# Kernel tuning notes

Hardware: AMD Instinct MI355X
Metric: run time of the kernel (lower is better)

## Reference

```python
import jax, jax.numpy as jnp
import numpy as np

SELF_LOOP_EPS = 0.5

def setup_inputs() -> dict:
    key = jax.random.key(0)
    k1, k2 = jax.random.split(key)
    spatial_nodes = jax.random.normal(k1, (16, 2048, 64), dtype=jnp.float32)
    temporal_nodes = jax.random.normal(k2, (16, 64, 64), dtype=jnp.float32)
    return {"spatial_nodes": spatial_nodes, "temporal_nodes": temporal_nodes}

def reference(spatial_nodes, temporal_nodes):
    # concat spatial and temporal node embeddings along the node axis: [B, N+T, D]
    node_embs = jnp.concatenate([spatial_nodes, temporal_nodes], axis=1)
    # batched gram matrix: [B, M, M], M = N+T
    adj = jnp.einsum('bnf,bmf->bnm', node_embs, node_embs)
    adj = jnp.tanh(jax.nn.relu(adj))
    M = adj.shape[1]
    # add scaled self loops
    adj = adj + jnp.eye(M, dtype=adj.dtype) * SELF_LOOP_EPS
    # the torch module additionally extracts per-batch nonzero (edge_index, edge_weight)
    # lists; that is data-dependent stream compaction. The dense adj (plus its nonzero
    # mask) carries the identical information in a jit-compatible fixed-shape form.
    return adj
```

## Files before the change

### kernel.cpp

```cpp
#include <hip/hip_runtime.h>
#include <hip/hip_fp16.h>


#define B_BATCH   16
#define N_SPATIAL 2048
#define T_TEMP    64
#define M_NODES   2112
#define D_FEAT    64
#define TILE      64
#define LDSK      72

#define GROUPS_PER_STRIP 17
#define WGS_PER_BATCH    (33 * GROUPS_PER_STRIP)
#define TOTAL_WGS        (WGS_PER_BATCH * B_BATCH)
#define WGS_PER_XCD      (TOTAL_WGS / 8)

typedef _Float16 f16x8 __attribute__((ext_vector_type(8)));
typedef float    f32x4 __attribute__((ext_vector_type(4)));

__device__ __forceinline__ f16x8 cvt2(const float4* p) {
    float4 a = p[0], c = p[1];
    f16x8 h;
    h[0] = (_Float16)a.x; h[1] = (_Float16)a.y;
    h[2] = (_Float16)a.z; h[3] = (_Float16)a.w;
    h[4] = (_Float16)c.x; h[5] = (_Float16)c.y;
    h[6] = (_Float16)c.z; h[7] = (_Float16)c.w;
    return h;
}

__global__ __launch_bounds__(256, 4)
void gram_tanh_mfma(const float* __restrict__ sp,
                    const float* __restrict__ tp,
                    float* __restrict__ out)
{
    const int lin = blockIdx.x;
    const int xcd = lin & 7;
    const int l   = lin >> 3;
    const int bo  = l / WGS_PER_BATCH;
    const int rr  = l - bo * WGS_PER_BATCH;
    const int ti  = rr / GROUPS_PER_STRIP;
    const int g   = rr - ti * GROUPS_PER_STRIP;
    const int b   = 2 * xcd + bo;
    const int tj0 = 2 * g;
    const bool have2 = (tj0 + 1 < 33);
    const int tj1 = have2 ? tj0 + 1 : 32;

    __shared__ __align__(16) _Float16 As[TILE][LDSK];
    __shared__ __align__(16) _Float16 Bs[2][TILE][LDSK];

    const int tid = threadIdx.x;

    {
        const int row = tid >> 2;
        const int kb  = (tid & 3) * 16;
        const float* srcA = (ti < 32)
            ? sp + ((size_t)b * N_SPATIAL + (size_t)ti * TILE) * D_FEAT
            : tp + (size_t)b * T_TEMP * D_FEAT;
        const float* srcB0 = (tj0 < 32)
            ? sp + ((size_t)b * N_SPATIAL + (size_t)tj0 * TILE) * D_FEAT
            : tp + (size_t)b * T_TEMP * D_FEAT;
        const float* srcB1 = (tj1 < 32)
            ? sp + ((size_t)b * N_SPATIAL + (size_t)tj1 * TILE) * D_FEAT
            : tp + (size_t)b * T_TEMP * D_FEAT;
        const float4* pa  = (const float4*)(srcA  + (size_t)row * D_FEAT + kb);
        const float4* pb0 = (const float4*)(srcB0 + (size_t)row * D_FEAT + kb);
        const float4* pb1 = (const float4*)(srcB1 + (size_t)row * D_FEAT + kb);

        *(f16x8*)&As[row][kb]        = cvt2(pa);
        *(f16x8*)&As[row][kb + 8]    = cvt2(pa + 2);
        *(f16x8*)&Bs[0][row][kb]     = cvt2(pb0);
        *(f16x8*)&Bs[0][row][kb + 8] = cvt2(pb0 + 2);
        *(f16x8*)&Bs[1][row][kb]     = cvt2(pb1);
        *(f16x8*)&Bs[1][row][kb + 8] = cvt2(pb1 + 2);
    }
    __syncthreads();

    const int wave = tid >> 6;
    const int lane = tid & 63;
    const int lr   = lane & 15;
    const int q    = lane >> 4;

    f32x4 acc[2][4];
    #pragma unroll
    for (int n = 0; n < 2; ++n)
        #pragma unroll
        for (int tt = 0; tt < 4; ++tt) acc[n][tt] = (f32x4){0.f, 0.f, 0.f, 0.f};

    #pragma unroll
    for (int s = 0; s < 2; ++s) {
        f16x8 afrag = *(const f16x8*)&As[wave * 16 + lr][s * 32 + q * 8];
        #pragma unroll
        for (int n = 0; n < 2; ++n) {
            #pragma unroll
            for (int tt = 0; tt < 4; ++tt) {
                f16x8 bfrag = *(const f16x8*)&Bs[n][tt * 16 + lr][s * 32 + q * 8];
                acc[n][tt] = __builtin_amdgcn_mfma_f32_16x16x32_f16(bfrag, afrag, acc[n][tt], 0, 0, 0);
            }
        }
    }

    #pragma unroll
    for (int n = 0; n < 2; ++n) {
        if (n == 1 && !have2) break;
        const int tjn = n ? tj1 : tj0;
        const bool diagT = (ti == tjn);
        const int r_loc = wave * 16 + lr;
        float* dst = out + (size_t)b * M_NODES * M_NODES
                         + (size_t)(ti * TILE + r_loc) * M_NODES
                         + (size_t)(tjn * TILE + q * 4);
        #pragma unroll
        for (int tt = 0; tt < 4; ++tt) {
            const int c_loc = tt * 16 + q * 4;
            float4 o;
            float* po = &o.x;
            #pragma unroll
            for (int i = 0; i < 4; ++i) {
                float x = fmaxf(acc[n][tt][i], 0.f);
                float e = __expf(2.f * x);
                float v = 1.f - 2.f * __builtin_amdgcn_rcpf(e + 1.f);
                if (diagT && (r_loc == c_loc + i)) v += 0.5f;
                po[i] = v;
            }
            *(float4*)(dst + tt * 16) = o;
        }
    }
}

extern "C" void kernel_launch(void* const* d_in, const int* in_sizes, int n_in,
                              void* d_out, int out_size, void* d_ws, size_t ws_size,
                              hipStream_t stream) {
    const float* sp = (const float*)d_in[0];
    const float* tp = (const float*)d_in[1];
    float* out = (float*)d_out;

    dim3 grid(TOTAL_WGS);
    dim3 block(256);
    hipLaunchKernelGGL(gram_tanh_mfma, grid, block, 0, stream, sp, tp, out);
}
```

Baseline: 290.6 us.

## Exploit Gram symmetry: compute upper-triangle tiles and mirror-write transposes

Remaps the grid so each batch launches only the workgroups covering the upper triangle of 64x64 tile pairs (305 instead of 561). Each off-diagonal tile is computed once and written twice: once directly, and once transposed via a second MFMA with swapped operands. This halves the global loads of input tiles and the number of workgroups, while the output write volume stays the same. The extra MFMAs and the uneven per-workgroup work (mirror tiles do double the stores) add cost in exchange, on a kernel that is mostly bound by output writes.

```diff
diff --git a/kernel.cpp b/kernel.cpp
--- a/kernel.cpp
+++ b/kernel.cpp
@@ -10,10 +10,10 @@
 #define TILE      64
 #define LDSK      72
 
-#define GROUPS_PER_STRIP 17
-#define WGS_PER_BATCH    (33 * GROUPS_PER_STRIP)
-#define TOTAL_WGS        (WGS_PER_BATCH * B_BATCH)
-#define WGS_PER_XCD      (TOTAL_WGS / 8)
+#define WGS_PER_BATCH 305
+#define TRI_BASE      272
+#define TOTAL_WGS     (WGS_PER_BATCH * B_BATCH)
+#define WGS_PER_XCD   (TOTAL_WGS / 8)
 
 typedef _Float16 f16x8 __attribute__((ext_vector_type(8)));
 typedef float    f32x4 __attribute__((ext_vector_type(4)));
@@ -28,6 +28,12 @@
     return h;
 }
 
+__device__ __forceinline__ float tanh_relu(float x) {
+    x = fmaxf(x, 0.f);
+    float e = __expf(2.f * x);
+    return 1.f - 2.f * __builtin_amdgcn_rcpf(e + 1.f);
+}
+
 __global__ __launch_bounds__(256, 4)
 void gram_tanh_mfma(const float* __restrict__ sp,
                     const float* __restrict__ tp,
@@ -36,14 +42,23 @@
     const int lin = blockIdx.x;
     const int xcd = lin & 7;
     const int l   = lin >> 3;
-    const int bo  = l / WGS_PER_BATCH;
-    const int rr  = l - bo * WGS_PER_BATCH;
-    const int ti  = rr / GROUPS_PER_STRIP;
-    const int g   = rr - ti * GROUPS_PER_STRIP;
+    const int bo  = (l >= WGS_PER_BATCH) ? 1 : 0;
+    const int t   = l - bo * WGS_PER_BATCH;
     const int b   = 2 * xcd + bo;
-    const int tj0 = 2 * g;
+
+    int c2, r;
+    if (t >= TRI_BASE) { c2 = 16; r = t - TRI_BASE; }
+    else {
+        c2 = (int)(0.5f * (sqrtf((float)(4 * t + 1)) - 1.f));
+        while ((c2 + 1) * (c2 + 2) <= t) ++c2;
+        while (c2 * (c2 + 1) > t) --c2;
+        r = t - c2 * (c2 + 1);
+    }
+    const int ti  = r;
+    const int tj0 = 2 * c2;
     const bool have2 = (tj0 + 1 < 33);
     const int tj1 = have2 ? tj0 + 1 : 32;
+    const bool do0 = (tj0 >= ti);
 
     __shared__ __align__(16) _Float16 As[TILE][LDSK];
     __shared__ __align__(16) _Float16 Bs[2][TILE][LDSK];
@@ -56,22 +71,26 @@
         const float* srcA = (ti < 32)
             ? sp + ((size_t)b * N_SPATIAL + (size_t)ti * TILE) * D_FEAT
             : tp + (size_t)b * T_TEMP * D_FEAT;
-        const float* srcB0 = (tj0 < 32)
-            ? sp + ((size_t)b * N_SPATIAL + (size_t)tj0 * TILE) * D_FEAT
-            : tp + (size_t)b * T_TEMP * D_FEAT;
-        const float* srcB1 = (tj1 < 32)
-            ? sp + ((size_t)b * N_SPATIAL + (size_t)tj1 * TILE) * D_FEAT
-            : tp + (size_t)b * T_TEMP * D_FEAT;
-        const float4* pa  = (const float4*)(srcA  + (size_t)row * D_FEAT + kb);
-        const float4* pb0 = (const float4*)(srcB0 + (size_t)row * D_FEAT + kb);
-        const float4* pb1 = (const float4*)(srcB1 + (size_t)row * D_FEAT + kb);
+        const float4* pa = (const float4*)(srcA + (size_t)row * D_FEAT + kb);
+        *(f16x8*)&As[row][kb]     = cvt2(pa);
+        *(f16x8*)&As[row][kb + 8] = cvt2(pa + 2);
 
-        *(f16x8*)&As[row][kb]        = cvt2(pa);
-        *(f16x8*)&As[row][kb + 8]    = cvt2(pa + 2);
-        *(f16x8*)&Bs[0][row][kb]     = cvt2(pb0);
-        *(f16x8*)&Bs[0][row][kb + 8] = cvt2(pb0 + 2);
-        *(f16x8*)&Bs[1][row][kb]     = cvt2(pb1);
-        *(f16x8*)&Bs[1][row][kb + 8] = cvt2(pb1 + 2);
+        if (do0) {
+            const float* srcB0 = (tj0 < 32)
+                ? sp + ((size_t)b * N_SPATIAL + (size_t)tj0 * TILE) * D_FEAT
+                : tp + (size_t)b * T_TEMP * D_FEAT;
+            const float4* pb0 = (const float4*)(srcB0 + (size_t)row * D_FEAT + kb);
+            *(f16x8*)&Bs[0][row][kb]     = cvt2(pb0);
+            *(f16x8*)&Bs[0][row][kb + 8] = cvt2(pb0 + 2);
+        }
+        if (have2) {
+            const float* srcB1 = (tj1 < 32)
+                ? sp + ((size_t)b * N_SPATIAL + (size_t)tj1 * TILE) * D_FEAT
+                : tp + (size_t)b * T_TEMP * D_FEAT;
+            const float4* pb1 = (const float4*)(srcB1 + (size_t)row * D_FEAT + kb);
+            *(f16x8*)&Bs[1][row][kb]     = cvt2(pb1);
+            *(f16x8*)&Bs[1][row][kb + 8] = cvt2(pb1 + 2);
+        }
     }
     __syncthreads();
 
@@ -80,48 +99,65 @@
     const int lr   = lane & 15;
     const int q    = lane >> 4;
 
-    f32x4 acc[2][4];
-    #pragma unroll
-    for (int n = 0; n < 2; ++n)
-        #pragma unroll
-        for (int tt = 0; tt < 4; ++tt) acc[n][tt] = (f32x4){0.f, 0.f, 0.f, 0.f};
+    float* const outb = out + (size_t)b * M_NODES * M_NODES;
 
     #pragma unroll
-    for (int s = 0; s < 2; ++s) {
-        f16x8 afrag = *(const f16x8*)&As[wave * 16 + lr][s * 32 + q * 8];
+    for (int n = 0; n < 2; ++n) {
+        if (n == 0 && !do0) continue;
+        if (n == 1 && !have2) continue;
+        const int tjn = n ? tj1 : tj0;
+        const bool mirror = (tjn > ti);
+        const bool diagT  = (tjn == ti);
+
+        f32x4 acc[4], accT[4];
         #pragma unroll
-        for (int n = 0; n < 2; ++n) {
+        for (int tt = 0; tt < 4; ++tt) {
+            acc[tt]  = (f32x4){0.f, 0.f, 0.f, 0.f};
+            accT[tt] = (f32x4){0.f, 0.f, 0.f, 0.f};
+        }
+
+        #pragma unroll
+        for (int s = 0; s < 2; ++s) {
+            f16x8 afrag = *(const f16x8*)&As[wave * 16 + lr][s * 32 + q * 8];
             #pragma unroll
             for (int tt = 0; tt < 4; ++tt) {
                 f16x8 bfrag = *(const f16x8*)&Bs[n][tt * 16 + lr][s * 32 + q * 8];
-                acc[n][tt] = __builtin_amdgcn_mfma_f32_16x16x32_f16(bfrag, afrag, acc[n][tt], 0, 0, 0);
+                acc[tt] = __builtin_amdgcn_mfma_f32_16x16x32_f16(bfrag, afrag, acc[tt], 0, 0, 0);
+                if (mirror)
+                    accT[tt] = __builtin_amdgcn_mfma_f32_16x16x32_f16(afrag, bfrag, accT[tt], 0, 0, 0);
             }
         }
-    }
 
-    #pragma unroll
-    for (int n = 0; n < 2; ++n) {
-        if (n == 1 && !have2) break;
-        const int tjn = n ? tj1 : tj0;
-        const bool diagT = (ti == tjn);
-        const int r_loc = wave * 16 + lr;
-        float* dst = out + (size_t)b * M_NODES * M_NODES
-                         + (size_t)(ti * TILE + r_loc) * M_NODES
-                         + (size_t)(tjn * TILE + q * 4);
-        #pragma unroll
-        for (int tt = 0; tt < 4; ++tt) {
-            const int c_loc = tt * 16 + q * 4;
-            float4 o;
-            float* po = &o.x;
+        {
+            const int r_loc = wave * 16 + lr;
+            float* dst = outb + (size_t)(ti * TILE + r_loc) * M_NODES
+                              + (size_t)(tjn * TILE + q * 4);
             #pragma unroll
-            for (int i = 0; i < 4; ++i) {
-                float x = fmaxf(acc[n][tt][i], 0.f);
-                float e = __expf(2.f * x);
-                float v = 1.f - 2.f * __builtin_amdgcn_rcpf(e + 1.f);
-                if (diagT && (r_loc == c_loc + i)) v += 0.5f;
-                po[i] = v;
+            for (int tt = 0; tt < 4; ++tt) {
+                const int c_loc = tt * 16 + q * 4;
+                float4 o;
+                float* po = &o.x;
+                #pragma unroll
+                for (int i = 0; i < 4; ++i) {
+                    float v = tanh_relu(acc[tt][i]);
+                    if (diagT && (r_loc == c_loc + i)) v += 0.5f;
+                    po[i] = v;
+                }
+                *(float4*)(dst + tt * 16) = o;
             }
-            *(float4*)(dst + tt * 16) = o;
+        }
+
+        if (mirror) {
+            const size_t cb = (size_t)(ti * TILE + wave * 16 + q * 4);
+            #pragma unroll
+            for (int tt = 0; tt < 4; ++tt) {
+                float* dstT = outb + (size_t)(tjn * TILE + tt * 16 + lr) * M_NODES + cb;
+                float4 o;
+                float* po = &o.x;
+                #pragma unroll
+                for (int i = 0; i < 4; ++i) po[i] = tanh_relu(accT[tt][i]);
+                *(float4*)dstT = o;
+            }
         }
     }
 }
```

Result: slower. 301.9 us (+3.9%).

## Convert to persistent kernel with register-prefetched next tile inputs

Applied to the files above, without the earlier changes.

Replaces the one-tile-per-workgroup grid with a persistent grid of 96 workgroups per XCD, each striding over its XCD's tile list. While the current tile is computed and stored, the fp32 inputs for the next tile are loaded into registers, overlapping global loads with MFMA work and output writes. It also lowers the occupancy hint from 4 to 3 to make room for the extra prefetch registers. The kernel is dominated by output writes, so the gain may be small, and fewer resident waves could reduce store throughput.

```diff
diff --git a/kernel.cpp b/kernel.cpp
--- a/kernel.cpp
+++ b/kernel.cpp
@@ -11,15 +11,15 @@
 #define LDSK      72
 
 #define GROUPS_PER_STRIP 17
-#define WGS_PER_BATCH    (33 * GROUPS_PER_STRIP)
-#define TOTAL_WGS        (WGS_PER_BATCH * B_BATCH)
-#define WGS_PER_XCD      (TOTAL_WGS / 8)
+#define TILES_PER_BATCH  (33 * GROUPS_PER_STRIP)
+#define TILES_PER_XCD    (2 * TILES_PER_BATCH)
+#define WGS_PER_XCD      96
+#define TOTAL_WGS        (WGS_PER_XCD * 8)
 
 typedef _Float16 f16x8 __attribute__((ext_vector_type(8)));
 typedef float    f32x4 __attribute__((ext_vector_type(4)));
 
-__device__ __forceinline__ f16x8 cvt2(const float4* p) {
-    float4 a = p[0], c = p[1];
+__device__ __forceinline__ f16x8 cvt2v(float4 a, float4 c) {
     f16x8 h;
     h[0] = (_Float16)a.x; h[1] = (_Float16)a.y;
     h[2] = (_Float16)a.z; h[3] = (_Float16)a.w;
@@ -28,101 +28,142 @@
     return h;
 }
 
-__global__ __launch_bounds__(256, 4)
+__device__ __forceinline__ float tanh_relu(float x) {
+    x = fmaxf(x, 0.f);
+    float e = __expf(2.f * x);
+    return 1.f - 2.f * __builtin_amdgcn_rcpf(e + 1.f);
+}
+
+__device__ __forceinline__ void tile_ptrs(int t, int xcd, int row, int kb,
+                                          const float* __restrict__ sp,
+                                          const float* __restrict__ tp,
+                                          const float4*& pa,
+                                          const float4*& pb0,
+                                          const float4*& pb1)
+{
+    const int bo  = (t >= TILES_PER_BATCH) ? 1 : 0;
+    const int rr  = t - bo * TILES_PER_BATCH;
+    const int ti  = rr / GROUPS_PER_STRIP;
+    const int g   = rr - ti * GROUPS_PER_STRIP;
+    const int b   = 2 * xcd + bo;
+    const int tj0 = 2 * g;
+    const int tj1 = (tj0 + 1 < 33) ? tj0 + 1 : 32;
+    const float* srcA = (ti < 32)
+        ? sp + ((size_t)b * N_SPATIAL + (size_t)ti * TILE) * D_FEAT
+        : tp + (size_t)b * T_TEMP * D_FEAT;
+    const float* srcB0 = (tj0 < 32)
+        ? sp + ((size_t)b * N_SPATIAL + (size_t)tj0 * TILE) * D_FEAT
+        : tp + (size_t)b * T_TEMP * D_FEAT;
+    const float* srcB1 = (tj1 < 32)
+        ? sp + ((size_t)b * N_SPATIAL + (size_t)tj1 * TILE) * D_FEAT
+        : tp + (size_t)b * T_TEMP * D_FEAT;
+    pa  = (const float4*)(srcA  + (size_t)row * D_FEAT + kb);
+    pb0 = (const float4*)(srcB0 + (size_t)row * D_FEAT + kb);
+    pb1 = (const float4*)(srcB1 + (size_t)row * D_FEAT + kb);
+}
+
+__global__ __launch_bounds__(256, 3)
 void gram_tanh_mfma(const float* __restrict__ sp,
                     const float* __restrict__ tp,
                     float* __restrict__ out)
 {
     const int lin = blockIdx.x;
     const int xcd = lin & 7;
-    const int l   = lin >> 3;
-    const int bo  = l / WGS_PER_BATCH;
-    const int rr  = l - bo * WGS_PER_BATCH;
-    const int ti  = rr / GROUPS_PER_STRIP;
-    const int g   = rr - ti * GROUPS_PER_STRIP;
-    const int b   = 2 * xcd + bo;
-    const int tj0 = 2 * g;
-    const bool have2 = (tj0 + 1 < 33);
-    const int tj1 = have2 ? tj0 + 1 : 32;
+    const int w   = lin >> 3;
 
     __shared__ __align__(16) _Float16 As[TILE][LDSK];
     __shared__ __align__(16) _Float16 Bs[2][TILE][LDSK];
 
-    const int tid = threadIdx.x;
-
-    {
-        const int row = tid >> 2;
-        const int kb  = (tid & 3) * 16;
-        const float* srcA = (ti < 32)
-            ? sp + ((size_t)b * N_SPATIAL + (size_t)ti * TILE) * D_FEAT
-            : tp + (size_t)b * T_TEMP * D_FEAT;
-        const float* srcB0 = (tj0 < 32)
-            ? sp + ((size_t)b * N_SPATIAL + (size_t)tj0 * TILE) * D_FEAT
-            : tp + (size_t)b * T_TEMP * D_FEAT;
-        const float* srcB1 = (tj1 < 32)
-            ? sp + ((size_t)b * N_SPATIAL + (size_t)tj1 * TILE) * D_FEAT
-            : tp + (size_t)b * T_TEMP * D_FEAT;
-        const float4* pa  = (const float4*)(srcA  + (size_t)row * D_FEAT + kb);
-        const float4* pb0 = (const float4*)(srcB0 + (size_t)row * D_FEAT + kb);
-        const float4* pb1 = (const float4*)(srcB1 + (size_t)row * D_FEAT + kb);
-
-        *(f16x8*)&As[row][kb]        = cvt2(pa);
-        *(f16x8*)&As[row][kb + 8]    = cvt2(pa + 2);
-        *(f16x8*)&Bs[0][row][kb]     = cvt2(pb0);
-        *(f16x8*)&Bs[0][row][kb + 8] = cvt2(pb0 + 2);
-        *(f16x8*)&Bs[1][row][kb]     = cvt2(pb1);
-        *(f16x8*)&Bs[1][row][kb + 8] = cvt2(pb1 + 2);
-    }
-    __syncthreads();
-
+    const int tid  = threadIdx.x;
+    const int row  = tid >> 2;
+    const int kb   = (tid & 3) * 16;
     const int wave = tid >> 6;
     const int lane = tid & 63;
     const int lr   = lane & 15;
     const int q    = lane >> 4;
 
-    f32x4 acc[2][4];
-    #pragma unroll
-    for (int n = 0; n < 2; ++n)
+    int t = w;
+    float4 ra[4], rb0[4], rb1[4];
+    {
+        const float4 *pa, *pb0, *pb1;
+        tile_ptrs(t, xcd, row, kb, sp, tp, pa, pb0, pb1);
         #pragma unroll
-        for (int tt = 0; tt < 4; ++tt) acc[n][tt] = (f32x4){0.f, 0.f, 0.f, 0.f};
+        for (int i = 0; i < 4; ++i) { ra[i] = pa[i]; rb0[i] = pb0[i]; rb1[i] = pb1[i]; }
+    }
 
-    #pragma unroll
-    for (int s = 0; s < 2; ++s) {
-        f16x8 afrag = *(const f16x8*)&As[wave * 16 + lr][s * 32 + q * 8];
+    for (;;) {
+        const int bo  = (t >= TILES_PER_BATCH) ? 1 : 0;
+        const int rr  = t - bo * TILES_PER_BATCH;
+        const int ti  = rr / GROUPS_PER_STRIP;
+        const int g   = rr - ti * GROUPS_PER_STRIP;
+        const int b   = 2 * xcd + bo;
+        const int tj0 = 2 * g;
+        const bool have2 = (tj0 + 1 < 33);
+        const int tj1 = have2 ? tj0 + 1 : 32;
+
+        __syncthreads();
+        *(f16x8*)&As[row][kb]        = cvt2v(ra[0],  ra[1]);
+        *(f16x8*)&As[row][kb + 8]    = cvt2v(ra[2],  ra[3]);
+        *(f16x8*)&Bs[0][row][kb]     = cvt2v(rb0[0], rb0[1]);
+        *(f16x8*)&Bs[0][row][kb + 8] = cvt2v(rb0[2], rb0[3]);
+        *(f16x8*)&Bs[1][row][kb]     = cvt2v(rb1[0], rb1[1]);
+        *(f16x8*)&Bs[1][row][kb + 8] = cvt2v(rb1[2], rb1[3]);
+        __syncthreads();
+
+        const int tn = t + WGS_PER_XCD;
+        const bool more = (tn < TILES_PER_XCD);
+        if (more) {
+            const float4 *pa, *pb0, *pb1;
+            tile_ptrs(tn, xcd, row, kb, sp, tp, pa, pb0, pb1);
+            #pragma unroll
+            for (int i = 0; i < 4; ++i) { ra[i] = pa[i]; rb0[i] = pb0[i]; rb1[i] = pb1[i]; }
+        }
+
+        f32x4 acc[2][4];
+        #pragma unroll
+        for (int n = 0; n < 2; ++n)
+            #pragma unroll
+            for (int tt = 0; tt < 4; ++tt) acc[n][tt] = (f32x4){0.f, 0.f, 0.f, 0.f};
+
+        #pragma unroll
+        for (int s = 0; s < 2; ++s) {
+            f16x8 afrag = *(const f16x8*)&As[wave * 16 + lr][s * 32 + q * 8];
+            #pragma unroll
+            for (int n = 0; n < 2; ++n) {
+                #pragma unroll
+                for (int tt = 0; tt < 4; ++tt) {
+                    f16x8 bfrag = *(const f16x8*)&Bs[n][tt * 16 + lr][s * 32 + q * 8];
+                    acc[n][tt] = __builtin_amdgcn_mfma_f32_16x16x32_f16(bfrag, afrag, acc[n][tt], 0, 0, 0);
+                }
+            }
+        }
+
         #pragma unroll
         for (int n = 0; n < 2; ++n) {
+            if (n == 1 && !have2) break;
+            const int tjn = n ? tj1 : tj0;
+            const bool diagT = (ti == tjn);
+            const int r_loc = wave * 16 + lr;
+            float* dst = out + (size_t)b * M_NODES * M_NODES
+                             + (size_t)(ti * TILE + r_loc) * M_NODES
+                             + (size_t)(tjn * TILE + q * 4);
             #pragma unroll
             for (int tt = 0; tt < 4; ++tt) {
-                f16x8 bfrag = *(const f16x8*)&Bs[n][tt * 16 + lr][s * 32 + q * 8];
-                acc[n][tt] = __builtin_amdgcn_mfma_f32_16x16x32_f16(bfrag, afrag, acc[n][tt], 0, 0, 0);
+                const int c_loc = tt * 16 + q * 4;
+                float4 o;
+                float* po = &o.x;
+                #pragma unroll
+                for (int i = 0; i < 4; ++i) {
+                    float v = tanh_relu(acc[n][tt][i]);
+                    if (diagT && (r_loc == c_loc + i)) v += 0.5f;
+                    po[i] = v;
+                }
+                *(float4*)(dst + tt * 16) = o;
             }
         }
-    }
 
-    #pragma unroll
-    for (int n = 0; n < 2; ++n) {
-        if (n == 1 && !have2) break;
-        const int tjn = n ? tj1 : tj0;
-        const bool diagT = (ti == tjn);
-        const int r_loc = wave * 16 + lr;
-        float* dst = out + (size_t)b * M_NODES * M_NODES
-                         + (size_t)(ti * TILE + r_loc) * M_NODES
-                         + (size_t)(tjn * TILE + q * 4);
-        #pragma unroll
-        for (int tt = 0; tt < 4; ++tt) {
-            const int c_loc = tt * 16 + q * 4;
-            float4 o;
-            float* po = &o.x;
-            #pragma unroll
-            for (int i = 0; i < 4; ++i) {
-                float x = fmaxf(acc[n][tt][i], 0.f);
-                float e = __expf(2.f * x);
-                float v = 1.f - 2.f * __builtin_amdgcn_rcpf(e + 1.f);
-                if (diagT && (r_loc == c_loc + i)) v += 0.5f;
-                po[i] = v;
-            }
-            *(float4*)(dst + tt * 16) = o;
-        }
+        if (!more) break;
+        t = tn;
     }
 }
 
```

New measurement: 301.8 us. 3.9% more time.
